# Kernel tuning notes

Hardware: AMD Instinct MI355X
Metric: run time of the kernel (lower is better)

Reference implementation:

```python
import jax, jax.numpy as jnp
import numpy as np

N = 50000
E = 800000
D_IN = 41
H = 192


def _glorot(key, shape):
    fan_in, fan_out = shape[0], shape[-1]
    lim = float(np.sqrt(6.0 / (fan_in + fan_out)))
    return jax.random.uniform(key, shape, minval=-lim, maxval=lim, dtype=jnp.float32)


def setup_inputs() -> dict:
    key = jax.random.key(0)
    ks = jax.random.split(key, 16)
    x = jax.random.normal(ks[0], (N, D_IN), dtype=jnp.float32)
    edge_index = jax.random.randint(ks[1], (2, E), 0, N, dtype=jnp.int64)
    Wc = jnp.stack([_glorot(jax.random.fold_in(ks[2], i), (H, H)) for i in range(4)])
    return {
        "x": x,
        "edge_index": edge_index,
        "W_in": _glorot(ks[3], (D_IN, H)), "b_in": jnp.zeros((H,), jnp.float32),
        "Wc": Wc, "bc": jnp.zeros((4, H), jnp.float32),
        "Wp1": _glorot(ks[4], (H, H)), "bp1": jnp.zeros((H,), jnp.float32),
        "Wp2": _glorot(ks[5], (H, H // 2)), "bp2": jnp.zeros((H // 2,), jnp.float32),
        "Wp3": _glorot(ks[6], (H // 2, 2)), "bp3": jnp.zeros((2,), jnp.float32),
        "Wr1": _glorot(ks[7], (H, H // 2)), "br1": jnp.zeros((H // 2,), jnp.float32),
        "Wr2": _glorot(ks[8], (H // 2, 1)), "br2": jnp.zeros((1,), jnp.float32),
    }


def reference(x, edge_index, W_in, b_in, Wc, bc, Wp1, bp1, Wp2, bp2, Wp3, bp3, Wr1, br1, Wr2, br2):
    n = x.shape[0]
    # GCN normalization with self-loops (PyG GCNConv default)
    loop = jnp.arange(n)
    src = jnp.concatenate([edge_index[0], loop])  # [E+N]
    dst = jnp.concatenate([edge_index[1], loop])
    deg = jax.ops.segment_sum(jnp.ones(src.shape, jnp.float32), dst, num_segments=n)
    dis = jax.lax.rsqrt(jnp.maximum(deg, 1.0))  # deg >= 1 due to self-loops
    coef = (dis[src] * dis[dst])[:, None]  # [E+N, 1]

    h = x @ W_in + b_in  # [N, H]
    for i in range(4):
        m = h @ Wc[i]                                   # linear transform
        agg = jax.ops.segment_sum(coef * m[src], dst, num_segments=n) + bc[i]
        h = h + jax.nn.relu(agg)                         # residual; dropout off (eval)

    # position head: 192 -> 192 -> 96 -> 2
    p = jax.nn.relu(h @ Wp1 + bp1)
    p = jax.nn.relu(p @ Wp2 + bp2)
    pos = p @ Wp3 + bp3  # [N, 2]

    # radius head: 192 -> 96 -> 1, constrained to (0, 1)
    r = jax.nn.relu(h @ Wr1 + br1)
    radius = jax.nn.sigmoid(r @ Wr2 + br2)  # [N, 1]

    # normalize position to unit circle and scale by radius (center=False)
    norm = jnp.sqrt(jnp.sum(pos * pos, axis=-1, keepdims=True) + 1e-8)
    coords = pos / norm * radius
    return coords
```

## Files before the change

### kernel.cpp

```cpp
#include <hip/hip_runtime.h>
#include <hip/hip_bf16.h>
#include <math.h>

#define N_NODES 50000
#define N_EDGES 800000
#define DIN 41
#define H 192
#define CAP 64
#define NTILES 3125
#define NPAIRS 1563

typedef __attribute__((ext_vector_type(8))) _Float16 f16x8;
typedef __attribute__((ext_vector_type(4))) float f32x4;


__global__ void k_count(const int* __restrict__ ei, int* __restrict__ cnt) {
    int e = blockIdx.x * blockDim.x + threadIdx.x;
    if (e < N_EDGES) atomicAdd(&cnt[ei[N_EDGES + e]], 1);
}

__global__ void k_dis(const int* __restrict__ cnt, float* __restrict__ dis) {
    int i = blockIdx.x * blockDim.x + threadIdx.x;
    if (i < N_NODES) dis[i] = rsqrtf((float)(cnt[i] + 1));
}

__global__ void k_fill(const int* __restrict__ ei, const float* __restrict__ dis,
                       int* __restrict__ cnt2, int2* __restrict__ adjp) {
    int e = blockIdx.x * blockDim.x + threadIdx.x;
    if (e >= N_EDGES) return;
    int s = ei[e];
    int d = ei[N_EDGES + e];
    int slot = atomicAdd(&cnt2[d], 1);
    if (slot < CAP) {
        adjp[d * CAP + slot] = make_int2(s, __float_as_int(dis[s] * dis[d]));
    }
}


__global__ void k_wprep(const float* __restrict__ Wc, const float* __restrict__ Wp1,
                        const float* __restrict__ Wp2, const float* __restrict__ Wr1,
                        _Float16* __restrict__ Wc_hi, _Float16* __restrict__ Wc_lo,
                        _Float16* __restrict__ Wp1_hi, _Float16* __restrict__ Wp1_lo,
                        _Float16* __restrict__ Wp2_hi, _Float16* __restrict__ Wp2_lo,
                        _Float16* __restrict__ Wr1_hi, _Float16* __restrict__ Wr1_lo) {
    int idx = blockIdx.x * blockDim.x + threadIdx.x;
    const float* src; _Float16 *hi, *lo; int K, N, off;
    if (idx < 147456) {
        int l = idx / 36864; off = idx - l * 36864;
        src = Wc + l * 36864; hi = Wc_hi + l * 36864; lo = Wc_lo + l * 36864; K = 192; N = 192;
    } else if (idx < 184320) {
        off = idx - 147456; src = Wp1; hi = Wp1_hi; lo = Wp1_lo; K = 192; N = 192;
    } else if (idx < 202752) {
        off = idx - 184320; src = Wp2; hi = Wp2_hi; lo = Wp2_lo; K = 192; N = 96;
    } else if (idx < 221184) {
        off = idx - 202752; src = Wr1; hi = Wr1_hi; lo = Wr1_lo; K = 192; N = 96;
    } else return;
    int n = off / K, k = off - n * K;
    float w = src[k * N + n];
    _Float16 h16 = (_Float16)w;
    hi[off] = h16;
    lo[off] = (_Float16)(w - (float)h16);
}


__global__ void k_in(const float* __restrict__ x, const float* __restrict__ W,
                     const float* __restrict__ b,
                     _Float16* __restrict__ hhi, _Float16* __restrict__ hlo) {
    __shared__ float xs[DIN];
    int i = blockIdx.x;
    int j = threadIdx.x;
    if (j < DIN) xs[j] = x[i * DIN + j];
    __syncthreads();
    float acc = b[j];
#pragma unroll
    for (int k = 0; k < DIN; ++k) acc = fmaf(xs[k], W[k * H + j], acc);
    _Float16 v16 = (_Float16)acc;
    hhi[i * H + j] = v16;
    hlo[i * H + j] = (_Float16)(acc - (float)v16);
}


template <int NT, bool RELU, bool BIAS, bool SPLIT_OUT, bool F16COPY>
__global__ __launch_bounds__(256) void k_mfma_gemm(
    const _Float16* __restrict__ Ahi, const _Float16* __restrict__ Alo,
    const _Float16* __restrict__ Bhi, const _Float16* __restrict__ Blo,
    const float* __restrict__ bias, float* __restrict__ Cf,
    _Float16* __restrict__ Chi, _Float16* __restrict__ Clo,
    _Float16* __restrict__ C16) {
    const int wave = threadIdx.x >> 6;
    const int lane = threadIdx.x & 63;
    const int q = blockIdx.x * 4 + wave;
    if (q >= NPAIRS) return;
    const int t0 = 2 * q;
    const int t1 = 2 * q + 1;
    const bool has2 = (t1 < NTILES);
    const int row16 = lane & 15;
    const int kb = lane >> 4;
    const long base0 = (long)t0 * 16;
    const long base1 = has2 ? (long)t1 * 16 : base0;

    f32x4 acc0[NT], acc1[NT];
#pragma unroll
    for (int nt = 0; nt < NT; ++nt) {
        acc0[nt] = (f32x4){0.f, 0.f, 0.f, 0.f};
        acc1[nt] = (f32x4){0.f, 0.f, 0.f, 0.f};
    }

#pragma unroll
    for (int kt = 0; kt < 6; ++kt) {
        const long aoff0 = (base0 + row16) * H + kb * 8 + kt * 32;
        const long aoff1 = (base1 + row16) * H + kb * 8 + kt * 32;
        f16x8 a0h = *(const f16x8*)(Ahi + aoff0);
        f16x8 a0l = *(const f16x8*)(Alo + aoff0);
        f16x8 a1h = *(const f16x8*)(Ahi + aoff1);
        f16x8 a1l = *(const f16x8*)(Alo + aoff1);
#pragma unroll
        for (int nt = 0; nt < NT; ++nt) {
            const long boff = (long)(nt * 16 + row16) * H + kb * 8 + kt * 32;
            f16x8 bhf = *(const f16x8*)(Bhi + boff);
            f16x8 blf = *(const f16x8*)(Blo + boff);
            acc0[nt] = __builtin_amdgcn_mfma_f32_16x16x32_f16(a0h, bhf, acc0[nt], 0, 0, 0);
            acc0[nt] = __builtin_amdgcn_mfma_f32_16x16x32_f16(a0l, bhf, acc0[nt], 0, 0, 0);
            acc0[nt] = __builtin_amdgcn_mfma_f32_16x16x32_f16(a0h, blf, acc0[nt], 0, 0, 0);
            acc1[nt] = __builtin_amdgcn_mfma_f32_16x16x32_f16(a1h, bhf, acc1[nt], 0, 0, 0);
            acc1[nt] = __builtin_amdgcn_mfma_f32_16x16x32_f16(a1l, bhf, acc1[nt], 0, 0, 0);
            acc1[nt] = __builtin_amdgcn_mfma_f32_16x16x32_f16(a1h, blf, acc1[nt], 0, 0, 0);
        }
    }

#pragma unroll
    for (int nt = 0; nt < NT; ++nt) {
        const int n = nt * 16 + row16;
        const float bs = BIAS ? bias[n] : 0.f;
#pragma unroll
        for (int r = 0; r < 4; ++r) {
            long node = base0 + kb * 4 + r;
            float v = acc0[nt][r] + bs;
            if (RELU) v = fmaxf(v, 0.f);
            if (SPLIT_OUT) {
                _Float16 v16 = (_Float16)v;
                Chi[node * (NT * 16) + n] = v16;
                Clo[node * (NT * 16) + n] = (_Float16)(v - (float)v16);
            } else {
                Cf[node * (NT * 16) + n] = v;
                if (F16COPY) C16[node * (NT * 16) + n] = (_Float16)v;
            }
        }
        if (has2) {
#pragma unroll
            for (int r = 0; r < 4; ++r) {
                long node = base1 + kb * 4 + r;
                float v = acc1[nt][r] + bs;
                if (RELU) v = fmaxf(v, 0.f);
                if (SPLIT_OUT) {
                    _Float16 v16 = (_Float16)v;
                    Chi[node * (NT * 16) + n] = v16;
                    Clo[node * (NT * 16) + n] = (_Float16)(v - (float)v16);
                } else {
                    Cf[node * (NT * 16) + n] = v;
                    if (F16COPY) C16[node * (NT * 16) + n] = (_Float16)v;
                }
            }
        }
    }
}


__global__ __launch_bounds__(256, 4) void k_agg(
    const float* __restrict__ m, const _Float16* __restrict__ m16,
    _Float16* __restrict__ hhi, _Float16* __restrict__ hlo,
    const int2* __restrict__ adjp,
    const int* __restrict__ cnt, const float* __restrict__ dis,
    const float* __restrict__ bc) {
    int gid = blockIdx.x * blockDim.x + threadIdx.x;
    int i = gid >> 6;
    int lane = threadIdx.x & 63;
    if (i >= N_NODES) return;

    float disi = dis[i];
    float selfc = disi * disi;
    const float* mi = m + (size_t)i * H;
    float a0 = selfc * mi[lane];
    float a1 = selfc * mi[lane + 64];
    float a2 = selfc * mi[lane + 128];

    int c = cnt[i];
    if (c > CAP) c = CAP;
    const int2* ap = adjp + (size_t)i * CAP;

    for (int e0 = 0; e0 < c; e0 += 16) {
        int off[16];
        float cf[16];
#pragma unroll
        for (int u = 0; u < 16; ++u) {
            bool ok = (e0 + u) < c;
            int idx = ok ? (e0 + u) : 0;
            int2 ent = ap[idx];
            off[u] = ent.x * H + lane;
            cf[u] = ok ? __int_as_float(ent.y) : 0.f;
        }
        float v0[16], v1[16], v2[16];
#pragma unroll
        for (int u = 0; u < 16; ++u) {
            v0[u] = (float)m16[off[u]];
            v1[u] = (float)m16[off[u] + 64];
            v2[u] = (float)m16[off[u] + 128];
        }
#pragma unroll
        for (int u = 0; u < 16; ++u) {
            a0 = fmaf(cf[u], v0[u], a0);
            a1 = fmaf(cf[u], v1[u], a1);
            a2 = fmaf(cf[u], v2[u], a2);
        }
    }

    size_t base = (size_t)i * H;
#pragma unroll
    for (int q = 0; q < 3; ++q) {
        size_t off = base + lane + q * 64;
        float agg = (q == 0) ? a0 : (q == 1) ? a1 : a2;
        float hv = (float)hhi[off] + (float)hlo[off] + fmaxf(agg + bc[lane + q * 64], 0.f);
        _Float16 t = (_Float16)hv;
        hhi[off] = t;
        hlo[off] = (_Float16)(hv - (float)t);
    }
}


__global__ void k_final(const float* __restrict__ p2, const float* __restrict__ r1,
                        const float* __restrict__ Wp3, const float* __restrict__ bp3,
                        const float* __restrict__ Wr2, const float* __restrict__ br2,
                        float* __restrict__ out) {
    int gid = blockIdx.x * blockDim.x + threadIdx.x;
    int i = gid >> 6;
    int lane = threadIdx.x & 63;
    if (i >= N_NODES) return;

    float s0 = 0.f, s1 = 0.f, sr = 0.f;
    for (int k = lane; k < 96; k += 64) {
        float pv = p2[(size_t)i * 96 + k];
        s0 = fmaf(pv, Wp3[k * 2 + 0], s0);
        s1 = fmaf(pv, Wp3[k * 2 + 1], s1);
        float rv = r1[(size_t)i * 96 + k];
        sr = fmaf(rv, Wr2[k], sr);
    }
#pragma unroll
    for (int off = 32; off > 0; off >>= 1) {
        s0 += __shfl_xor(s0, off);
        s1 += __shfl_xor(s1, off);
        sr += __shfl_xor(sr, off);
    }
    if (lane == 0) {
        s0 += bp3[0];
        s1 += bp3[1];
        float rad = 1.f / (1.f + expf(-(sr + br2[0])));
        float norm = sqrtf(s0 * s0 + s1 * s1 + 1e-8f);
        float inv = rad / norm;
        out[(size_t)i * 2 + 0] = s0 * inv;
        out[(size_t)i * 2 + 1] = s1 * inv;
    }
}


extern "C" void kernel_launch(void* const* d_in, const int* in_sizes, int n_in,
                              void* d_out, int out_size, void* d_ws, size_t ws_size,
                              hipStream_t stream) {
    (void)in_sizes; (void)n_in; (void)out_size; (void)ws_size;

    const float* x    = (const float*)d_in[0];
    const int*   ei   = (const int*)d_in[1];
    const float* W_in = (const float*)d_in[2];
    const float* b_in = (const float*)d_in[3];
    const float* Wc   = (const float*)d_in[4];
    const float* bc   = (const float*)d_in[5];
    const float* Wp1  = (const float*)d_in[6];
    const float* bp1  = (const float*)d_in[7];
    const float* Wp2  = (const float*)d_in[8];
    const float* bp2  = (const float*)d_in[9];
    const float* Wp3  = (const float*)d_in[10];
    const float* bp3  = (const float*)d_in[11];
    const float* Wr1  = (const float*)d_in[12];
    const float* br1  = (const float*)d_in[13];
    const float* Wr2  = (const float*)d_in[14];
    const float* br2  = (const float*)d_in[15];
    float* out = (float*)d_out;

    char* ws = (char*)d_ws;
    float*     m        = (float*)    (ws + 0);
    float*     p2buf    = (float*)    (ws + 0);
    float*     r1buf    = (float*)    (ws + 19200000);
    _Float16*  m16      = (_Float16*) (ws + 38400000);
    _Float16*  h_hi     = (_Float16*) (ws + 57600000);
    _Float16*  h_lo     = (_Float16*) (ws + 76800000);
    _Float16*  p1_hi    = (_Float16*) (ws + 96000000);
    _Float16*  p1_lo    = (_Float16*) (ws + 115200000);
    float*     dis      = (float*)    (ws + 134400000);
    int*       cnt      = (int*)      (ws + 134600000);
    int*       cnt2     = (int*)      (ws + 134800000);
    int2*      adjp     = (int2*)     (ws + 135000000);
    _Float16*  Wc_hi    = (_Float16*) (ws + 160600000);
    _Float16*  Wc_lo    = (_Float16*) (ws + 160894912);
    _Float16*  Wp1_hi   = (_Float16*) (ws + 161189824);
    _Float16*  Wp1_lo   = (_Float16*) (ws + 161263552);
    _Float16*  Wp2_hi   = (_Float16*) (ws + 161337280);
    _Float16*  Wp2_lo   = (_Float16*) (ws + 161374144);
    _Float16*  Wr1_hi   = (_Float16*) (ws + 161411008);
    _Float16*  Wr1_lo   = (_Float16*) (ws + 161447872);

    hipMemsetAsync(cnt, 0, 400000, stream);

    const int EB = (N_EDGES + 255) / 256;
    const int NB = (N_NODES + 255) / 256;

    k_count<<<EB, 256, 0, stream>>>(ei, cnt);
    k_dis<<<NB, 256, 0, stream>>>(cnt, dis);
    k_fill<<<EB, 256, 0, stream>>>(ei, dis, cnt2, adjp);

    k_wprep<<<(221184 + 255) / 256, 256, 0, stream>>>(
        Wc, Wp1, Wp2, Wr1, Wc_hi, Wc_lo, Wp1_hi, Wp1_lo,
        Wp2_hi, Wp2_lo, Wr1_hi, Wr1_lo);

    k_in<<<N_NODES, H, 0, stream>>>(x, W_in, b_in, h_hi, h_lo);

    const int GB2 = (NPAIRS + 3) / 4;
    for (int l = 0; l < 4; ++l) {
        k_mfma_gemm<12, false, false, false, true><<<GB2, 256, 0, stream>>>(
            h_hi, h_lo, Wc_hi + (size_t)l * H * H, Wc_lo + (size_t)l * H * H,
            nullptr, m, nullptr, nullptr, m16);
        k_agg<<<N_NODES / 4, 256, 0, stream>>>(m, m16, h_hi, h_lo, adjp,
                                               cnt, dis, bc + (size_t)l * H);
    }

    k_mfma_gemm<12, true, true, true, false><<<GB2, 256, 0, stream>>>(
        h_hi, h_lo, Wp1_hi, Wp1_lo, bp1, nullptr, p1_hi, p1_lo, nullptr);
    k_mfma_gemm<6, true, true, false, false><<<GB2, 256, 0, stream>>>(
        p1_hi, p1_lo, Wp2_hi, Wp2_lo, bp2, p2buf, nullptr, nullptr, nullptr);
    k_mfma_gemm<6, true, true, false, false><<<GB2, 256, 0, stream>>>(
        h_hi, h_lo, Wr1_hi, Wr1_lo, br1, r1buf, nullptr, nullptr, nullptr);

    k_final<<<N_NODES / 4, 256, 0, stream>>>(p2buf, r1buf, Wp3, bp3, Wr2, br2, out);
}
```

Before: 802.6 us.

## Stage GEMM weight tiles in double-buffered swizzled LDS shared across waves

Result: faster. 656.6 us (-18.2%).

```diff
diff --git a/kernel.cpp b/kernel.cpp
--- a/kernel.cpp
+++ b/kernel.cpp
@@ -87,10 +87,15 @@
     const float* __restrict__ bias, float* __restrict__ Cf,
     _Float16* __restrict__ Chi, _Float16* __restrict__ Clo,
     _Float16* __restrict__ C16) {
+    constexpr int NROWS = NT * 16;
+    constexpr int CHUNKS = NROWS * 4;
+    constexpr int PT = (CHUNKS + 255) / 256;
+    __shared__ _Float16 ldsB[2][2][NROWS * 32];
+
     const int wave = threadIdx.x >> 6;
     const int lane = threadIdx.x & 63;
-    const int q = blockIdx.x * 4 + wave;
-    if (q >= NPAIRS) return;
+    int q = blockIdx.x * 4 + wave;
+    if (q >= NPAIRS) q = NPAIRS - 1;
     const int t0 = 2 * q;
     const int t1 = 2 * q + 1;
     const bool has2 = (t1 < NTILES);
@@ -99,6 +104,32 @@
     const long base0 = (long)t0 * 16;
     const long base1 = has2 ? (long)t1 * 16 : base0;
 
+    f16x8 sh[PT], sl[PT];
+    auto LOADC = [&](int kt) {
+#pragma unroll
+        for (int u = 0; u < PT; ++u) {
+            int c = (int)threadIdx.x + u * 256;
+            if (c < CHUNKS) {
+                int n = c >> 2, p = c & 3;
+                long g = (long)n * H + kt * 32 + p * 8;
+                sh[u] = *(const f16x8*)(Bhi + g);
+                sl[u] = *(const f16x8*)(Blo + g);
+            }
+        }
+    };
+    auto STOREC = [&](int buf) {
+#pragma unroll
+        for (int u = 0; u < PT; ++u) {
+            int c = (int)threadIdx.x + u * 256;
+            if (c < CHUNKS) {
+                int n = c >> 2, p = c & 3;
+                int sp = p ^ ((n >> 1) & 3);
+                *(f16x8*)((char*)&ldsB[buf][0][0] + n * 64 + sp * 16) = sh[u];
+                *(f16x8*)((char*)&ldsB[buf][1][0] + n * 64 + sp * 16) = sl[u];
+            }
+        }
+    };
+
     f32x4 acc0[NT], acc1[NT];
 #pragma unroll
     for (int nt = 0; nt < NT; ++nt) {
@@ -106,19 +137,31 @@
         acc1[nt] = (f32x4){0.f, 0.f, 0.f, 0.f};
     }
 
+    LOADC(0);
+    STOREC(0);
+    __syncthreads();
+
+    const int swz = (row16 >> 1) & 3;
+
 #pragma unroll
     for (int kt = 0; kt < 6; ++kt) {
+        const int buf = kt & 1;
+        if (kt < 5) LOADC(kt + 1);
+
         const long aoff0 = (base0 + row16) * H + kb * 8 + kt * 32;
         const long aoff1 = (base1 + row16) * H + kb * 8 + kt * 32;
         f16x8 a0h = *(const f16x8*)(Ahi + aoff0);
         f16x8 a0l = *(const f16x8*)(Alo + aoff0);
         f16x8 a1h = *(const f16x8*)(Ahi + aoff1);
         f16x8 a1l = *(const f16x8*)(Alo + aoff1);
+
+        const char* bh = (const char*)&ldsB[buf][0][0];
+        const char* bl = (const char*)&ldsB[buf][1][0];
 #pragma unroll
         for (int nt = 0; nt < NT; ++nt) {
-            const long boff = (long)(nt * 16 + row16) * H + kb * 8 + kt * 32;
-            f16x8 bhf = *(const f16x8*)(Bhi + boff);
-            f16x8 blf = *(const f16x8*)(Blo + boff);
+            const int off = (nt * 16 + row16) * 64 + (((kb ^ swz)) * 16);
+            f16x8 bhf = *(const f16x8*)(bh + off);
+            f16x8 blf = *(const f16x8*)(bl + off);
             acc0[nt] = __builtin_amdgcn_mfma_f32_16x16x32_f16(a0h, bhf, acc0[nt], 0, 0, 0);
             acc0[nt] = __builtin_amdgcn_mfma_f32_16x16x32_f16(a0l, bhf, acc0[nt], 0, 0, 0);
             acc0[nt] = __builtin_amdgcn_mfma_f32_16x16x32_f16(a0h, blf, acc0[nt], 0, 0, 0);
@@ -126,6 +169,9 @@
             acc1[nt] = __builtin_amdgcn_mfma_f32_16x16x32_f16(a1l, bhf, acc1[nt], 0, 0, 0);
             acc1[nt] = __builtin_amdgcn_mfma_f32_16x16x32_f16(a1h, blf, acc1[nt], 0, 0, 0);
         }
+
+        if (kt < 5) STOREC(buf ^ 1);
+        __syncthreads();
     }
 
 #pragma unroll
```
